# Performance work log

Measured on AMD Instinct MI355X. Metric: run time of the kernel, lower is better.

Reference implementation:

```python
import jax, jax.numpy as jnp
import numpy as np

D_MODEL = 2048
N_HEADS = 16
N_KV = 8
HEAD_DIM = 128
G = N_HEADS // N_KV  # q heads per kv head
SCALE = float(np.sqrt(HEAD_DIM))
B, T = 2, 2048


def setup_inputs() -> dict:
    key = jax.random.key(0)
    k1, k2, k3, k4, k5 = jax.random.split(key, 5)
    s = 0.02
    return {
        "x": jax.random.normal(k1, (B, T, D_MODEL), dtype=jnp.float32),
        "Wq": jax.random.normal(k2, (N_HEADS * HEAD_DIM, D_MODEL), dtype=jnp.float32) * s,
        "Wk": jax.random.normal(k3, (N_KV * HEAD_DIM, D_MODEL), dtype=jnp.float32) * s,
        "Wv": jax.random.normal(k4, (N_KV * HEAD_DIM, D_MODEL), dtype=jnp.float32) * s,
        "Wo": jax.random.normal(k5, (D_MODEL, N_HEADS * HEAD_DIM), dtype=jnp.float32) * s,
    }


def reference(x, Wq, Wk, Wv, Wo):
    # Projections (nn.Linear: y = x @ W.T), dropout prob = 0 so omitted.
    b, t, _ = x.shape
    q = (x @ Wq.T).reshape(b, t, N_KV, G, HEAD_DIM)   # (B,T,Hkv,G,d)
    k = (x @ Wk.T).reshape(b, t, N_KV, HEAD_DIM)      # (B,T,Hkv,d)
    v = (x @ Wv.T).reshape(b, t, N_KV, HEAD_DIM)
    # GQA: each kv head shared by G query heads (equivalent to repeat_interleave).
    scores = jnp.einsum('btghd,bsgd->bghts', q, k) / SCALE  # (B,Hkv,G,T,T)
    attn = jax.nn.softmax(scores, axis=-1)
    out = jnp.einsum('bghts,bsgd->btghd', attn, v)          # (B,T,Hkv,G,d)
    out = out.reshape(b, t, N_HEADS * HEAD_DIM)
    return out @ Wo.T
```

## Files before the change

### kernel.cpp

```cpp
#include <hip/hip_runtime.h>
#include <hip/hip_bf16.h>

typedef __attribute__((ext_vector_type(8))) short short8;
typedef __attribute__((ext_vector_type(4))) float floatx4;

__device__ inline unsigned short f2bf(float f) {
    unsigned int u = __float_as_uint(f);
    u += 0x7fffu + ((u >> 16) & 1u);
    return (unsigned short)(u >> 16);
}

__device__ inline unsigned int pk_bf16(float lo, float hi) {
    __hip_bfloat162 h = __float22bfloat162_rn(float2{lo, hi});
    unsigned int u;
    __builtin_memcpy(&u, &h, 4);
    return u;
}

__global__ void cast_all_kernel(const float* __restrict__ x,
                                const float* __restrict__ wq,
                                const float* __restrict__ wk,
                                const float* __restrict__ wv,
                                const float* __restrict__ wo,
                                unsigned short* __restrict__ xb,
                                unsigned short* __restrict__ wqkb,
                                unsigned short* __restrict__ wvb,
                                unsigned short* __restrict__ wob) {
    const float C2 = 0.08838834764831845f * 1.4426950408889634f;
    int bid = blockIdx.x;
    const float* src;
    unsigned short* dst;
    int base;
    float sc = 1.0f;
    if (bid < 8192)       { src = x;  dst = xb;             base = bid; }
    else if (bid < 12288) { src = wq; dst = wqkb;           base = bid - 8192; sc = C2; }
    else if (bid < 14336) { src = wk; dst = wqkb + 4194304; base = bid - 12288; }
    else if (bid < 16384) { src = wv; dst = wvb;            base = bid - 14336; }
    else                  { src = wo; dst = wob;            base = bid - 16384; }
    int i = base * 256 + threadIdx.x;
    float4 v = ((const float4*)src)[i];
    ushort4 o;
    o.x = f2bf(v.x * sc); o.y = f2bf(v.y * sc);
    o.z = f2bf(v.z * sc); o.w = f2bf(v.w * sc);
    ((ushort4*)dst)[i] = o;
}

template <int OUT_BF16>
__device__ __forceinline__ void gemm_bt64_body(
        const unsigned short* __restrict__ A,
        const unsigned short* __restrict__ B,
        void* __restrict__ Cp, int K, int ldc, int m0, int n0,
        unsigned short* sA, unsigned short* sB) {
    const int tid  = threadIdx.x;
    const int wave = tid >> 6;
    const int lane = tid & 63;
    const int l16  = lane & 15;
    const int lq   = lane >> 4;
    const int wm   = (wave >> 1) * 64;
    const int wn   = (wave & 1) * 64;

    floatx4 acc[4][4] = {};

    const unsigned short* gA[4];
    const unsigned short* gB[4];
#pragma unroll
    for (int i = 0; i < 4; i++) {
        int c   = wave * 4 + i;
        int row = c * 8 + (lane >> 3);
        int chs = (lane & 7) ^ (row & 7);
        gA[i] = A + (size_t)(m0 + row) * K + chs * 8;
        gB[i] = B + (size_t)(n0 + row) * K + chs * 8;
    }

    for (int k0 = 0; k0 < K; k0 += 64) {
        __syncthreads();
#pragma unroll
        for (int i = 0; i < 4; i++) {
            int c = wave * 4 + i;
            __builtin_amdgcn_global_load_lds(
                (const __attribute__((address_space(1))) void*)gA[i],
                (__attribute__((address_space(3))) void*)(sA + c * 512), 16, 0, 0);
            gA[i] += 64;
            __builtin_amdgcn_global_load_lds(
                (const __attribute__((address_space(1))) void*)gB[i],
                (__attribute__((address_space(3))) void*)(sB + c * 512), 16, 0, 0);
            gB[i] += 64;
        }
        __syncthreads();

        short8 af[2][4], bfr[2][4];
#pragma unroll
        for (int ks = 0; ks < 2; ks++) {
            int slot = (ks * 4 + lq) ^ (l16 & 7);
#pragma unroll
            for (int mb = 0; mb < 4; mb++)
                af[ks][mb] = *(const short8*)(sA + (wm + mb * 16 + l16) * 64 + slot * 8);
#pragma unroll
            for (int nb = 0; nb < 4; nb++)
                bfr[ks][nb] = *(const short8*)(sB + (wn + nb * 16 + l16) * 64 + slot * 8);
        }
#pragma unroll
        for (int ks = 0; ks < 2; ks++)
#pragma unroll
            for (int mb = 0; mb < 4; mb++)
#pragma unroll
                for (int nb = 0; nb < 4; nb++)
                    acc[mb][nb] = __builtin_amdgcn_mfma_f32_16x16x32_bf16(
                        af[ks][mb], bfr[ks][nb], acc[mb][nb], 0, 0, 0);
    }

#pragma unroll
    for (int mb = 0; mb < 4; mb++)
#pragma unroll
        for (int nb = 0; nb < 4; nb++)
#pragma unroll
            for (int r = 0; r < 4; r++) {
                int row = m0 + wm + mb * 16 + lq * 4 + r;
                int col = n0 + wn + nb * 16 + l16;
                if (OUT_BF16)
                    ((unsigned short*)Cp)[(size_t)row * ldc + col] = f2bf(acc[mb][nb][r]);
                else
                    ((float*)Cp)[(size_t)row * ldc + col] = acc[mb][nb][r];
            }
}

__global__ __launch_bounds__(256) void gemm_qkv_kernel(
        const unsigned short* __restrict__ x_bf,
        const unsigned short* __restrict__ Wqk,
        const unsigned short* __restrict__ Wv,
        unsigned short* __restrict__ QKb,
        unsigned short* __restrict__ Vtb) {
    __shared__ __align__(16) unsigned short sA[128 * 64];
    __shared__ __align__(16) unsigned short sB[128 * 64];
    const int bid = blockIdx.x;
    if (bid < 768) {
        gemm_bt64_body<1>(x_bf, Wqk, QKb, 2048, 3072,
                          (bid / 24) * 128, (bid % 24) * 128, sA, sB);
    } else {
        int t = bid - 768;
        gemm_bt64_body<1>(Wv, x_bf, Vtb, 2048, 4096,
                          (t / 32) * 128, (t % 32) * 128, sA, sB);
    }
}

__global__ __launch_bounds__(256) void gemm_o_kernel(
        const unsigned short* __restrict__ A,
        const unsigned short* __restrict__ B,
        float* __restrict__ C) {
    __shared__ __align__(16) unsigned short sA[128 * 64];
    __shared__ __align__(16) unsigned short sB[128 * 64];
    gemm_bt64_body<0>(A, B, C, 2048, 2048,
                      blockIdx.y * 128, blockIdx.x * 128, sA, sB);
}

__global__ __launch_bounds__(256, 2) void flash_kernel(
        const unsigned short* __restrict__ QK,
        const unsigned short* __restrict__ Vt,
        unsigned short* __restrict__ O) {
    __shared__ __align__(16) unsigned short smem[40960];

    const int tid  = threadIdx.x;
    const int wave = tid >> 6;
    const int lane = tid & 63;
    const int l16  = lane & 15;
    const int lq   = lane >> 4;
    const int qt   = blockIdx.x;
    const int bh   = blockIdx.y;
    const int b    = bh >> 4;
    const int h    = bh & 15;
    const int kvh  = h >> 1;
    const size_t tokbase = (size_t)b * 2048 + qt * 128 + wave * 32;

    short8 qf[2][4];
#pragma unroll
    for (int qb = 0; qb < 2; qb++) {
        const unsigned short* qp =
            QK + (tokbase + qb * 16 + l16) * 3072 + h * 128 + lq * 8;
#pragma unroll
        for (int c = 0; c < 4; c++) qf[qb][c] = *(const short8*)(qp + c * 32);
    }

    const unsigned short* gKe =
        QK + ((size_t)b * 2048 + wave * 16 + lq) * 3072 + 2048 + kvh * 128 +
        (l16 ^ lq) * 8;
    const unsigned short* gKo =
        QK + ((size_t)b * 2048 + wave * 16 + 4 + lq) * 3072 + 2048 + kvh * 128 +
        (l16 ^ (lq + 4)) * 8;
    const unsigned short* gV0 =
        Vt + (size_t)(kvh * 128 + wave * 32 + (lane >> 3)) * 4096 +
        (size_t)b * 2048 + ((lane & 7) ^ (lane >> 3)) * 8;

#define STAGE_KT(sKd, sVd)                                                     \
    do {                                                                       \
        _Pragma("unroll")                                                      \
        for (int i = 0; i < 4; i++) {                                          \
            const unsigned short* gk =                                         \
                ((i & 1) ? gKo : gKe) + (i >> 1) * 24576;                      \
            __builtin_amdgcn_global_load_lds(                                  \
                (const __attribute__((address_space(1))) void*)gk,             \
                (__attribute__((address_space(3))) void*)((sKd) +              \
                                                          (wave * 4 + i) * 512),\
                16, 0, 0);                                                     \
            __builtin_amdgcn_global_load_lds(                                  \
                (const __attribute__((address_space(1))) void*)(gV0 +          \
                                                               i * 32768),     \
                (__attribute__((address_space(3))) void*)((sVd) +              \
                                                          (wave * 4 + i) * 512),\
                16, 0, 0);                                                     \
        }                                                                      \
        gKe += 196608; gKo += 196608; gV0 += 64;                               \
    } while (0)

    unsigned short* pB = smem + 32768 + wave * 2048;

    floatx4 oacc[2][8] = {};
    float l_run[2] = {0.0f, 0.0f};

    STAGE_KT(smem, smem + 16384);
    asm volatile("s_waitcnt vmcnt(0)" ::: "memory");
    __builtin_amdgcn_s_barrier();
    asm volatile("" ::: "memory");

    for (int kt = 0; kt < 32; kt++) {
        const int cur = kt & 1;
        const unsigned short* sKc = smem + cur * 8192;
        const unsigned short* sVc = smem + 16384 + cur * 8192;
        if (kt < 31) {
            unsigned short* sKn = smem + (cur ^ 1) * 8192;
            unsigned short* sVn = smem + 16384 + (cur ^ 1) * 8192;
            STAGE_KT(sKn, sVn);
        }

#pragma unroll
        for (int kb = 0; kb < 2; kb++) {
            floatx4 sacc[2] = {};
#pragma unroll
            for (int c = 0; c < 4; c++) {
                short8 kf = *(const short8*)(
                    sKc + (kb * 16 + l16) * 128 + (((c * 4 + lq) ^ (l16 & 7)) * 8));
#pragma unroll
                for (int qb = 0; qb < 2; qb++)
                    sacc[qb] = __builtin_amdgcn_mfma_f32_16x16x32_bf16(
                        kf, qf[qb][c], sacc[qb], 0, 0, 0);
            }
#pragma unroll
            for (int qb = 0; qb < 2; qb++) {
                float p0 = __builtin_exp2f(sacc[qb][0]);
                float p1 = __builtin_exp2f(sacc[qb][1]);
                float p2 = __builtin_exp2f(sacc[qb][2]);
                float p3 = __builtin_exp2f(sacc[qb][3]);
                l_run[qb] += (p0 + p1) + (p2 + p3);
                int row = qb * 16 + l16;
                uint2 u;
                u.x = pk_bf16(p0, p1);
                u.y = pk_bf16(p2, p3);
                *(uint2*)(pB + row * 64 +
                          (((kb * 2 + (lq >> 1)) ^ (row & 7)) * 8) +
                          (lq & 1) * 4) = u;
            }
        }
        asm volatile("s_waitcnt lgkmcnt(0)" ::: "memory");

        short8 pf0[2];
#pragma unroll
        for (int qb = 0; qb < 2; qb++) {
            int row = qb * 16 + l16;
            pf0[qb] = *(const short8*)(pB + row * 64 +
                                       ((lq ^ (row & 7)) * 8));
        }

        __builtin_amdgcn_s_setprio(1);
#pragma unroll
        for (int nb = 0; nb < 8; nb++) {
            short8 vf = *(const short8*)(
                sVc + (nb * 16 + l16) * 64 + ((lq ^ (l16 & 7)) * 8));
#pragma unroll
            for (int qb = 0; qb < 2; qb++)
                oacc[qb][nb] = __builtin_amdgcn_mfma_f32_16x16x32_bf16(
                    vf, pf0[qb], oacc[qb][nb], 0, 0, 0);
        }
        __builtin_amdgcn_s_setprio(0);

#pragma unroll
        for (int kb = 2; kb < 4; kb++) {
            floatx4 sacc[2] = {};
#pragma unroll
            for (int c = 0; c < 4; c++) {
                short8 kf = *(const short8*)(
                    sKc + (kb * 16 + l16) * 128 + (((c * 4 + lq) ^ (l16 & 7)) * 8));
#pragma unroll
                for (int qb = 0; qb < 2; qb++)
                    sacc[qb] = __builtin_amdgcn_mfma_f32_16x16x32_bf16(
                        kf, qf[qb][c], sacc[qb], 0, 0, 0);
            }
#pragma unroll
            for (int qb = 0; qb < 2; qb++) {
                float p0 = __builtin_exp2f(sacc[qb][0]);
                float p1 = __builtin_exp2f(sacc[qb][1]);
                float p2 = __builtin_exp2f(sacc[qb][2]);
                float p3 = __builtin_exp2f(sacc[qb][3]);
                l_run[qb] += (p0 + p1) + (p2 + p3);
                int row = qb * 16 + l16;
                uint2 u;
                u.x = pk_bf16(p0, p1);
                u.y = pk_bf16(p2, p3);
                *(uint2*)(pB + row * 64 +
                          (((kb * 2 + (lq >> 1)) ^ (row & 7)) * 8) +
                          (lq & 1) * 4) = u;
            }
        }
        asm volatile("s_waitcnt lgkmcnt(0)" ::: "memory");

        short8 pf1[2];
#pragma unroll
        for (int qb = 0; qb < 2; qb++) {
            int row = qb * 16 + l16;
            pf1[qb] = *(const short8*)(pB + row * 64 +
                                       (((4 + lq) ^ (row & 7)) * 8));
        }

        __builtin_amdgcn_s_setprio(1);
#pragma unroll
        for (int nb = 0; nb < 8; nb++) {
            short8 vf = *(const short8*)(
                sVc + (nb * 16 + l16) * 64 + (((4 + lq) ^ (l16 & 7)) * 8));
#pragma unroll
            for (int qb = 0; qb < 2; qb++)
                oacc[qb][nb] = __builtin_amdgcn_mfma_f32_16x16x32_bf16(
                    vf, pf1[qb], oacc[qb][nb], 0, 0, 0);
        }
        __builtin_amdgcn_s_setprio(0);

        asm volatile("s_waitcnt vmcnt(0)" ::: "memory");
        __builtin_amdgcn_s_barrier();
        asm volatile("" ::: "memory");
    }
#undef STAGE_KT

#pragma unroll
    for (int qb = 0; qb < 2; qb++) {
        float l = l_run[qb];
        l += __shfl_xor(l, 16);
        l += __shfl_xor(l, 32);
        float inv = 1.0f / l;
        size_t row = (tokbase + qb * 16 + l16) * 2048 + h * 128;
#pragma unroll
        for (int nb = 0; nb < 8; nb++) {
            uint2 u;
            u.x = pk_bf16(oacc[qb][nb][0] * inv, oacc[qb][nb][1] * inv);
            u.y = pk_bf16(oacc[qb][nb][2] * inv, oacc[qb][nb][3] * inv);
            *(uint2*)(O + row + nb * 16 + lq * 4) = u;
        }
    }
}

extern "C" void kernel_launch(void* const* d_in, const int* in_sizes, int n_in,
                              void* d_out, int out_size, void* d_ws, size_t ws_size,
                              hipStream_t stream) {
    const float* x  = (const float*)d_in[0];
    const float* Wq = (const float*)d_in[1];
    const float* Wk = (const float*)d_in[2];
    const float* Wv = (const float*)d_in[3];
    const float* Wo = (const float*)d_in[4];

    char* ws = (char*)d_ws;
    unsigned short* x_bf   = (unsigned short*)(ws);
    unsigned short* Wqk_bf = (unsigned short*)(ws + 16777216);
    unsigned short* Wv_bf  = (unsigned short*)(ws + 29360128);
    unsigned short* Wo_bf  = (unsigned short*)(ws + 33554432);
    unsigned short* QKb    = (unsigned short*)(ws + 41943040);
    unsigned short* Vtb    = (unsigned short*)(ws + 67108864);
    unsigned short* Ob     = (unsigned short*)(ws + 75497472);

    cast_all_kernel<<<dim3(20480), 256, 0, stream>>>(
        x, Wq, Wk, Wv, Wo, x_bf, Wqk_bf, Wv_bf, Wo_bf);

    gemm_qkv_kernel<<<dim3(1024), 256, 0, stream>>>(x_bf, Wqk_bf, Wv_bf, QKb, Vtb);

    flash_kernel<<<dim3(16, 32), 256, 0, stream>>>(QKb, Vtb, Ob);

    gemm_o_kernel<<<dim3(16, 32), 256, 0, stream>>>(Ob, Wo_bf, (float*)d_out);
}
```

Before: 326.6 us.

## Rewrite projection GEMMs as 128x256 tiles with triple-buffered LDS pipeline

```diff
diff --git a/kernel.cpp b/kernel.cpp
--- a/kernel.cpp
+++ b/kernel.cpp
@@ -46,68 +46,118 @@
 }
 
 template <int OUT_BF16>
-__device__ __forceinline__ void gemm_bt64_body(
+__device__ __forceinline__ void gemm256_body(
         const unsigned short* __restrict__ A,
         const unsigned short* __restrict__ B,
-        void* __restrict__ Cp, int K, int ldc, int m0, int n0,
-        unsigned short* sA, unsigned short* sB) {
+        void* __restrict__ Cp, int ldc, int m0, int n0,
+        unsigned short* sAb, unsigned short* sBb) {
     const int tid  = threadIdx.x;
     const int wave = tid >> 6;
     const int lane = tid & 63;
     const int l16  = lane & 15;
     const int lq   = lane >> 4;
-    const int wm   = (wave >> 1) * 64;
-    const int wn   = (wave & 1) * 64;
+    const int wm   = (wave >> 2) * 64;
+    const int wn   = (wave & 3) * 64;
 
     floatx4 acc[4][4] = {};
 
-    const unsigned short* gA[4];
+    const unsigned short* gA[2];
     const unsigned short* gB[4];
 #pragma unroll
-    for (int i = 0; i < 4; i++) {
-        int c   = wave * 4 + i;
+    for (int i = 0; i < 2; i++) {
+        int c   = wave * 2 + i;
         int row = c * 8 + (lane >> 3);
         int chs = (lane & 7) ^ (row & 7);
-        gA[i] = A + (size_t)(m0 + row) * K + chs * 8;
-        gB[i] = B + (size_t)(n0 + row) * K + chs * 8;
-    }
-
-    for (int k0 = 0; k0 < K; k0 += 64) {
-        __syncthreads();
-#pragma unroll
-        for (int i = 0; i < 4; i++) {
-            int c = wave * 4 + i;
-            __builtin_amdgcn_global_load_lds(
-                (const __attribute__((address_space(1))) void*)gA[i],
-                (__attribute__((address_space(3))) void*)(sA + c * 512), 16, 0, 0);
-            gA[i] += 64;
-            __builtin_amdgcn_global_load_lds(
-                (const __attribute__((address_space(1))) void*)gB[i],
-                (__attribute__((address_space(3))) void*)(sB + c * 512), 16, 0, 0);
-            gB[i] += 64;
-        }
-        __syncthreads();
-
-        short8 af[2][4], bfr[2][4];
-#pragma unroll
-        for (int ks = 0; ks < 2; ks++) {
-            int slot = (ks * 4 + lq) ^ (l16 & 7);
-#pragma unroll
-            for (int mb = 0; mb < 4; mb++)
-                af[ks][mb] = *(const short8*)(sA + (wm + mb * 16 + l16) * 64 + slot * 8);
-#pragma unroll
-            for (int nb = 0; nb < 4; nb++)
-                bfr[ks][nb] = *(const short8*)(sB + (wn + nb * 16 + l16) * 64 + slot * 8);
-        }
-#pragma unroll
-        for (int ks = 0; ks < 2; ks++)
-#pragma unroll
-            for (int mb = 0; mb < 4; mb++)
-#pragma unroll
-                for (int nb = 0; nb < 4; nb++)
-                    acc[mb][nb] = __builtin_amdgcn_mfma_f32_16x16x32_bf16(
-                        af[ks][mb], bfr[ks][nb], acc[mb][nb], 0, 0, 0);
-    }
+        gA[i] = A + (size_t)(m0 + row) * 2048 + chs * 8;
+    }
+#pragma unroll
+    for (int u = 0; u < 2; u++)
+#pragma unroll
+        for (int i = 0; i < 2; i++) {
+            int c   = u * 16 + wave * 2 + i;
+            int row = c * 8 + (lane >> 3);
+            int chs = (lane & 7) ^ (row & 7);
+            gB[u * 2 + i] = B + (size_t)(n0 + row) * 2048 + chs * 8;
+        }
+
+#define STG_A(slot)                                                            \
+    do {                                                                       \
+        _Pragma("unroll")                                                      \
+        for (int i = 0; i < 2; i++) {                                          \
+            __builtin_amdgcn_global_load_lds(                                  \
+                (const __attribute__((address_space(1))) void*)gA[i],          \
+                (__attribute__((address_space(3))) void*)(sAb + (slot) * 8192 +\
+                                                          (wave * 2 + i) * 512),\
+                16, 0, 0);                                                     \
+            gA[i] += 64;                                                       \
+        }                                                                      \
+    } while (0)
+#define STG_B(slot, u)                                                         \
+    do {                                                                       \
+        _Pragma("unroll")                                                      \
+        for (int i = 0; i < 2; i++) {                                          \
+            __builtin_amdgcn_global_load_lds(                                  \
+                (const __attribute__((address_space(1))) void*)gB[(u) * 2 + i],\
+                (__attribute__((address_space(3))) void*)(sBb + (slot) * 16384 \
+                                                  + ((u) * 16 + wave * 2 + i) * 512),\
+                16, 0, 0);                                                     \
+            gB[(u) * 2 + i] += 64;                                             \
+        }                                                                      \
+    } while (0)
+
+#define COMPUTE_KS(sA, sB, ks)                                                 \
+    do {                                                                       \
+        short8 af[4], bfr[4];                                                  \
+        int slot = ((ks) * 4 + lq) ^ (l16 & 7);                                \
+        _Pragma("unroll")                                                      \
+        for (int mb = 0; mb < 4; mb++)                                         \
+            af[mb] = *(const short8*)((sA) + (wm + mb * 16 + l16) * 64 +       \
+                                      slot * 8);                               \
+        _Pragma("unroll")                                                      \
+        for (int nb = 0; nb < 4; nb++)                                         \
+            bfr[nb] = *(const short8*)((sB) + (wn + nb * 16 + l16) * 64 +      \
+                                       slot * 8);                              \
+        __builtin_amdgcn_s_setprio(1);                                         \
+        _Pragma("unroll")                                                      \
+        for (int mb = 0; mb < 4; mb++)                                         \
+            _Pragma("unroll")                                                  \
+            for (int nb = 0; nb < 4; nb++)                                     \
+                acc[mb][nb] = __builtin_amdgcn_mfma_f32_16x16x32_bf16(         \
+                    af[mb], bfr[nb], acc[mb][nb], 0, 0, 0);                    \
+        __builtin_amdgcn_s_setprio(0);                                         \
+    } while (0)
+
+    STG_A(0); STG_B(0, 0); STG_B(0, 1);
+    STG_A(1); STG_B(1, 0); STG_B(1, 1);
+
+    int sc = 0;
+    for (int t = 0; t < 31; t++) {
+        int sn = sc + 2; if (sn >= 3) sn -= 3;
+        asm volatile("s_waitcnt vmcnt(6)" ::: "memory");
+        __builtin_amdgcn_s_barrier();
+        asm volatile("" ::: "memory");
+        const unsigned short* sA = sAb + sc * 8192;
+        const unsigned short* sB = sBb + sc * 16384;
+        if (t < 30) { STG_A(sn); STG_B(sn, 0); }
+        COMPUTE_KS(sA, sB, 0);
+        __builtin_amdgcn_s_barrier();
+        asm volatile("" ::: "memory");
+        if (t < 30) STG_B(sn, 1);
+        COMPUTE_KS(sA, sB, 1);
+        sc = sc + 1; if (sc >= 3) sc -= 3;
+    }
+    asm volatile("s_waitcnt vmcnt(0)" ::: "memory");
+    __builtin_amdgcn_s_barrier();
+    asm volatile("" ::: "memory");
+    {
+        const unsigned short* sA = sAb + sc * 8192;
+        const unsigned short* sB = sBb + sc * 16384;
+        COMPUTE_KS(sA, sB, 0);
+        COMPUTE_KS(sA, sB, 1);
+    }
+#undef STG_A
+#undef STG_B
+#undef COMPUTE_KS
 
 #pragma unroll
     for (int mb = 0; mb < 4; mb++)
@@ -124,33 +174,33 @@
             }
 }
 
-__global__ __launch_bounds__(256) void gemm_qkv_kernel(
+__global__ __launch_bounds__(512, 1) void gemm_qkv_kernel(
         const unsigned short* __restrict__ x_bf,
         const unsigned short* __restrict__ Wqk,
         const unsigned short* __restrict__ Wv,
         unsigned short* __restrict__ QKb,
         unsigned short* __restrict__ Vtb) {
-    __shared__ __align__(16) unsigned short sA[128 * 64];
-    __shared__ __align__(16) unsigned short sB[128 * 64];
+    __shared__ __align__(16) unsigned short sAb[3 * 8192];
+    __shared__ __align__(16) unsigned short sBb[3 * 16384];
     const int bid = blockIdx.x;
-    if (bid < 768) {
-        gemm_bt64_body<1>(x_bf, Wqk, QKb, 2048, 3072,
-                          (bid / 24) * 128, (bid % 24) * 128, sA, sB);
+    if (bid < 384) {
+        gemm256_body<1>(x_bf, Wqk, QKb, 3072,
+                        (bid / 12) * 128, (bid % 12) * 256, sAb, sBb);
     } else {
-        int t = bid - 768;
-        gemm_bt64_body<1>(Wv, x_bf, Vtb, 2048, 4096,
-                          (t / 32) * 128, (t % 32) * 128, sA, sB);
-    }
-}
-
-__global__ __launch_bounds__(256) void gemm_o_kernel(
+        int t = bid - 384;
+        gemm256_body<1>(Wv, x_bf, Vtb, 4096,
+                        (t / 16) * 128, (t % 16) * 256, sAb, sBb);
+    }
+}
+
+__global__ __launch_bounds__(512, 1) void gemm_o_kernel(
         const unsigned short* __restrict__ A,
         const unsigned short* __restrict__ B,
         float* __restrict__ C) {
-    __shared__ __align__(16) unsigned short sA[128 * 64];
-    __shared__ __align__(16) unsigned short sB[128 * 64];
-    gemm_bt64_body<0>(A, B, C, 2048, 2048,
-                      blockIdx.y * 128, blockIdx.x * 128, sA, sB);
+    __shared__ __align__(16) unsigned short sAb[3 * 8192];
+    __shared__ __align__(16) unsigned short sBb[3 * 16384];
+    gemm256_body<0>(A, B, C, 2048,
+                    blockIdx.y * 128, blockIdx.x * 256, sAb, sBb);
 }
 
 __global__ __launch_bounds__(256, 2) void flash_kernel(
@@ -375,9 +425,9 @@
     cast_all_kernel<<<dim3(20480), 256, 0, stream>>>(
         x, Wq, Wk, Wv, Wo, x_bf, Wqk_bf, Wv_bf, Wo_bf);
 
-    gemm_qkv_kernel<<<dim3(1024), 256, 0, stream>>>(x_bf, Wqk_bf, Wv_bf, QKb, Vtb);
+    gemm_qkv_kernel<<<dim3(512), 512, 0, stream>>>(x_bf, Wqk_bf, Wv_bf, QKb, Vtb);
 
     flash_kernel<<<dim3(16, 32), 256, 0, stream>>>(QKb, Vtb, Ob);
 
-    gemm_o_kernel<<<dim3(16, 32), 256, 0, stream>>>(Ob, Wo_bf, (float*)d_out);
-}
+    gemm_o_kernel<<<dim3(8, 32), 512, 0, stream>>>(Ob, Wo_bf, (float*)d_out);
+}
```

Measured after the change: 369.9 us. 13.2% more time.

## Rewrite QKV projection GEMM with 256x256 tiles and 4-stage direct-to-LDS pipeline

Applied to the files above, without the earlier changes.

```diff
diff --git a/kernel.cpp b/kernel.cpp
--- a/kernel.cpp
+++ b/kernel.cpp
@@ -46,6 +46,147 @@
 }
 
 template <int OUT_BF16>
+__device__ __forceinline__ void gemm256_body(
+        const unsigned short* __restrict__ A,
+        const unsigned short* __restrict__ B,
+        void* __restrict__ Cp, int ldc, int m0, int n0,
+        unsigned short* sL) {
+    const int tid  = threadIdx.x;
+    const int wave = tid >> 6;
+    const int lane = tid & 63;
+    const int l16  = lane & 15;
+    const int lq   = lane >> 4;
+    const int wm   = (wave >> 2) * 128;
+    const int wn   = (wave & 3) * 64;
+    const int kx   = lq ^ (l16 & 3);
+
+    floatx4 acc[8][4] = {};
+
+    const unsigned short* gA[2];
+    const unsigned short* gB[2];
+#pragma unroll
+    for (int i = 0; i < 2; i++) {
+        int c   = wave * 2 + i;
+        int row = c * 16 + (lane >> 2);
+        int g   = (lane & 3) ^ (row & 3);
+        gA[i] = A + (size_t)(m0 + row) * 2048 + g * 8;
+        gB[i] = B + (size_t)(n0 + row) * 2048 + g * 8;
+    }
+
+#define STG_A32(slot)                                                          \
+    do {                                                                       \
+        _Pragma("unroll")                                                      \
+        for (int i = 0; i < 2; i++) {                                          \
+            __builtin_amdgcn_global_load_lds(                                  \
+                (const __attribute__((address_space(1))) void*)gA[i],          \
+                (__attribute__((address_space(3))) void*)(sL + (slot) * 16384 +\
+                                                          (wave * 2 + i) * 512),\
+                16, 0, 0);                                                     \
+            gA[i] += 32;                                                       \
+        }                                                                      \
+    } while (0)
+#define STG_B32(slot)                                                          \
+    do {                                                                       \
+        _Pragma("unroll")                                                      \
+        for (int i = 0; i < 2; i++) {                                          \
+            __builtin_amdgcn_global_load_lds(                                  \
+                (const __attribute__((address_space(1))) void*)gB[i],          \
+                (__attribute__((address_space(3))) void*)(sL + (slot) * 16384 +\
+                                                  8192 + (wave * 2 + i) * 512),\
+                16, 0, 0);                                                     \
+            gB[i] += 32;                                                       \
+        }                                                                      \
+    } while (0)
+
+    STG_A32(0); STG_B32(0);
+    STG_A32(1); STG_B32(1);
+
+    for (int t = 0; t < 64; t++) {
+        const int sc = t & 3;
+        const int sn = (t + 2) & 3;
+        if (t < 63) asm volatile("s_waitcnt vmcnt(4)" ::: "memory");
+        else        asm volatile("s_waitcnt vmcnt(0)" ::: "memory");
+        __builtin_amdgcn_s_barrier();
+        asm volatile("" ::: "memory");
+
+        const unsigned short* sAc = sL + sc * 16384;
+        const unsigned short* sBc = sAc + 8192;
+        short8 af[4], bf[4];
+
+#pragma unroll
+        for (int mb = 0; mb < 4; mb++)
+            af[mb] = *(const short8*)(sAc + (wm + mb * 16 + l16) * 32 + kx * 8);
+#pragma unroll
+        for (int nb = 0; nb < 4; nb++)
+            bf[nb] = *(const short8*)(sBc + (wn + nb * 16 + l16) * 32 + kx * 8);
+        if (t < 62) STG_A32(sn);
+        __builtin_amdgcn_s_barrier();
+        asm volatile("s_waitcnt lgkmcnt(0)" ::: "memory");
+        __builtin_amdgcn_sched_barrier(0);
+        __builtin_amdgcn_s_setprio(1);
+#pragma unroll
+        for (int mb = 0; mb < 4; mb++)
+#pragma unroll
+            for (int nb = 0; nb < 4; nb++)
+                acc[mb][nb] = __builtin_amdgcn_mfma_f32_16x16x32_bf16(
+                    af[mb], bf[nb], acc[mb][nb], 0, 0, 0);
+        __builtin_amdgcn_s_setprio(0);
+        __builtin_amdgcn_s_barrier();
+        asm volatile("" ::: "memory");
+
+#pragma unroll
+        for (int mb = 0; mb < 4; mb++)
+            af[mb] = *(const short8*)(sAc + (wm + 64 + mb * 16 + l16) * 32 + kx * 8);
+        if (t < 62) STG_B32(sn);
+        __builtin_amdgcn_s_barrier();
+        asm volatile("s_waitcnt lgkmcnt(0)" ::: "memory");
+        __builtin_amdgcn_sched_barrier(0);
+        __builtin_amdgcn_s_setprio(1);
+#pragma unroll
+        for (int mb = 0; mb < 4; mb++)
+#pragma unroll
+            for (int nb = 0; nb < 4; nb++)
+                acc[4 + mb][nb] = __builtin_amdgcn_mfma_f32_16x16x32_bf16(
+                    af[mb], bf[nb], acc[4 + mb][nb], 0, 0, 0);
+        __builtin_amdgcn_s_setprio(0);
+    }
+#undef STG_A32
+#undef STG_B32
+
+#pragma unroll
+    for (int mb = 0; mb < 8; mb++)
+#pragma unroll
+        for (int nb = 0; nb < 4; nb++)
+#pragma unroll
+            for (int r = 0; r < 4; r++) {
+                int row = m0 + wm + mb * 16 + lq * 4 + r;
+                int col = n0 + wn + nb * 16 + l16;
+                if (OUT_BF16)
+                    ((unsigned short*)Cp)[(size_t)row * ldc + col] = f2bf(acc[mb][nb][r]);
+                else
+                    ((float*)Cp)[(size_t)row * ldc + col] = acc[mb][nb][r];
+            }
+}
+
+__global__ __launch_bounds__(512, 1) void gemm_qkv_kernel(
+        const unsigned short* __restrict__ x_bf,
+        const unsigned short* __restrict__ Wqk,
+        const unsigned short* __restrict__ Wv,
+        unsigned short* __restrict__ QKb,
+        unsigned short* __restrict__ Vtb) {
+    __shared__ __align__(16) unsigned short sL[4 * 16384];
+    const int bid = blockIdx.x;
+    if (bid < 192) {
+        gemm256_body<1>(x_bf, Wqk, QKb, 3072,
+                        (bid / 12) * 256, (bid % 12) * 256, sL);
+    } else {
+        int t = bid - 192;
+        gemm256_body<1>(Wv, x_bf, Vtb, 4096,
+                        (t / 16) * 256, (t % 16) * 256, sL);
+    }
+}
+
+template <int OUT_BF16>
 __device__ __forceinline__ void gemm_bt64_body(
         const unsigned short* __restrict__ A,
         const unsigned short* __restrict__ B,
@@ -122,25 +263,6 @@
                 else
                     ((float*)Cp)[(size_t)row * ldc + col] = acc[mb][nb][r];
             }
-}
-
-__global__ __launch_bounds__(256) void gemm_qkv_kernel(
-        const unsigned short* __restrict__ x_bf,
-        const unsigned short* __restrict__ Wqk,
-        const unsigned short* __restrict__ Wv,
-        unsigned short* __restrict__ QKb,
-        unsigned short* __restrict__ Vtb) {
-    __shared__ __align__(16) unsigned short sA[128 * 64];
-    __shared__ __align__(16) unsigned short sB[128 * 64];
-    const int bid = blockIdx.x;
-    if (bid < 768) {
-        gemm_bt64_body<1>(x_bf, Wqk, QKb, 2048, 3072,
-                          (bid / 24) * 128, (bid % 24) * 128, sA, sB);
-    } else {
-        int t = bid - 768;
-        gemm_bt64_body<1>(Wv, x_bf, Vtb, 2048, 4096,
-                          (t / 32) * 128, (t % 32) * 128, sA, sB);
-    }
 }
 
 __global__ __launch_bounds__(256) void gemm_o_kernel(
@@ -375,7 +497,7 @@
     cast_all_kernel<<<dim3(20480), 256, 0, stream>>>(
         x, Wq, Wk, Wv, Wo, x_bf, Wqk_bf, Wv_bf, Wo_bf);
 
-    gemm_qkv_kernel<<<dim3(1024), 256, 0, stream>>>(x_bf, Wqk_bf, Wv_bf, QKb, Vtb);
+    gemm_qkv_kernel<<<dim3(256), 512, 0, stream>>>(x_bf, Wqk_bf, Wv_bf, QKb, Vtb);
 
     flash_kernel<<<dim3(16, 32), 256, 0, stream>>>(QKb, Vtb, Ob);
 
```

Measured after the change: 316.4 us. -3.1%, faster.
